# Kernel tuning notes

Hardware: AMD Instinct MI355X
Metric: run time of the kernel (lower is better)

Reference implementation:

```python
import jax, jax.numpy as jnp
import numpy as np

B, T, C, H = 4, 2048, 1024, 16
D = C // H  # head_dim = 64


def setup_inputs() -> dict:
    key = jax.random.key(0)
    ks = jax.random.split(key, 4)
    scale = 1.0 / np.sqrt(C)
    return {
        "x": jax.random.normal(ks[0], (B, T, C), dtype=jnp.float32),
        "attn_mask": jnp.ones((B, T), dtype=jnp.int32),
        "W_qkv": jax.random.normal(ks[1], (C, 3 * C), dtype=jnp.float32) * scale,
        "b_qkv": jnp.zeros((3 * C,), dtype=jnp.float32),
        "W_proj": jax.random.normal(ks[2], (C, C), dtype=jnp.float32) * scale,
        "b_proj": jnp.zeros((C,), dtype=jnp.float32),
    }


def reference(x, attn_mask, W_qkv, b_qkv, W_proj, b_proj):
    b, t, c = x.shape
    qkv = x @ W_qkv + b_qkv                      # (B,T,3C)
    q, k, v = jnp.split(qkv, 3, axis=-1)
    # b t (h d) -> b h t d
    q = q.reshape(b, t, H, D).transpose(0, 2, 1, 3)
    k = k.reshape(b, t, H, D).transpose(0, 2, 1, 3)
    v = v.reshape(b, t, H, D).transpose(0, 2, 1, 3)
    att = jnp.einsum("bhtd,bhsd->bhts", q, k) / jnp.sqrt(jnp.float32(D))
    causal = jnp.tril(jnp.ones((t, t), dtype=bool))[None, None]       # (1,1,T,T)
    pad = (attn_mask[:, None, None, :t] != 0)                         # (B,1,1,T)
    att = jnp.where(causal & pad, att, -jnp.inf)
    att = jax.nn.softmax(att, axis=-1)
    y = jnp.einsum("bhts,bhsd->bhtd", att, v)   # (B,H,T,D)
    y = y.transpose(0, 2, 1, 3).reshape(b, t, c)
    return y @ W_proj + b_proj
```

## Files before the change

kernel.cpp:

```cpp
#include <hip/hip_runtime.h>
#include <math.h>

#define B_ 4
#define T_ 2048
#define C_ 1024
#define H_ 16
#define D_ 64
#define M_ (B_*T_)
#define N1_ (3*C_)

typedef __attribute__((ext_vector_type(8))) short bf16x8;
typedef __attribute__((ext_vector_type(4))) short bf16x4;
typedef __attribute__((ext_vector_type(4))) float f32x4;
typedef __attribute__((ext_vector_type(16))) float f32x16;

__device__ __forceinline__ short f2bf(float f){
  union { float f; unsigned u; } v; v.f = f;
  unsigned r = (v.u + 0x7fffu + ((v.u >> 16) & 1u)) >> 16;
  return (short)r;
}

__device__ __forceinline__ unsigned cvtpk(float lo, float hi){
  unsigned r;
  asm("v_cvt_pk_bf16_f32 %0, %1, %2" : "=v"(r) : "v"(lo), "v"(hi));
  return r;
}

__device__ __forceinline__ void plswap(unsigned &a, unsigned &b){
  asm volatile("v_permlane32_swap_b32 %0, %1" : "+v"(a), "+v"(b));
}
__device__ __forceinline__ float xhalf_add(float x){
  unsigned a = __float_as_uint(x), b = a;
  asm volatile("v_permlane32_swap_b32 %0, %1" : "+v"(a), "+v"(b));
  return __uint_as_float(a) + __uint_as_float(b);
}

__device__ __forceinline__ void gll16(const void* g, void* l){
  __builtin_amdgcn_global_load_lds((const __attribute__((address_space(1))) void*)g,
                                   (__attribute__((address_space(3))) void*)l, 16, 0, 0);
}

__global__ __launch_bounds__(256) void convx(const float* __restrict__ x, short* __restrict__ xb, int n){
  int i = (blockIdx.x*256 + threadIdx.x)*8;
  if (i >= n) return;
  float4 a = *(const float4*)(x+i), b = *(const float4*)(x+i+4);
  bf16x8 o;
  o[0]=f2bf(a.x); o[1]=f2bf(a.y); o[2]=f2bf(a.z); o[3]=f2bf(a.w);
  o[4]=f2bf(b.x); o[5]=f2bf(b.y); o[6]=f2bf(b.z); o[7]=f2bf(b.w);
  *(bf16x8*)(xb+i) = o;
}

__global__ __launch_bounds__(256) void transw(const float* __restrict__ W, short* __restrict__ Wt, int K, int N){
  __shared__ float tl[64][72];
  int tid = threadIdx.x;
  int n0 = blockIdx.x*64, k0 = blockIdx.y*64;
  #pragma unroll
  for (int i=0;i<4;i++){
    int row = (tid>>4) + i*16;
    int col4 = (tid&15)*4;
    float4 v = *(const float4*)&W[(size_t)(k0+row)*N + n0 + col4];
    *(float4*)&tl[row][col4] = v;
  }
  __syncthreads();
  #pragma unroll
  for (int i=0;i<2;i++){
    int nr = (tid>>3) + i*32;
    int ch = tid&7;
    bf16x8 o;
    #pragma unroll
    for (int e=0;e<8;e++) o[e] = f2bf(tl[ch*8+e][nr]);
    *(bf16x8*)&Wt[(size_t)(n0+nr)*K + k0 + ch*8] = o;
  }
}

template<int OUTBF>
__global__ __launch_bounds__(256) void gemm_bt(const short* __restrict__ A, const short* __restrict__ Bt,
           const float* __restrict__ bias, short* __restrict__ outb, float* __restrict__ outf,
           int M, int N, int K)
{
  __shared__ short As[128*32];
  __shared__ short Bs[128*32];
  const int tid = threadIdx.x;
  const int wv = tid >> 6, ln = tid & 63;
  const int lnr = ln & 15, lg = ln >> 4;
  const int m0 = blockIdx.y * 128, n0 = blockIdx.x * 128;
  const int wm = wv >> 1, wn = wv & 1;
  f32x4 acc[4][4];
  #pragma unroll
  for(int i=0;i<4;i++)
    #pragma unroll
    for(int j=0;j<4;j++) acc[i][j] = (f32x4){0.f,0.f,0.f,0.f};

  for (int k0 = 0; k0 < K; k0 += 32){
    #pragma unroll
    for (int c = 0; c < 2; c++){
      int i = c*256 + tid;
      gll16(A  + (size_t)(m0 + (i>>2))*K + k0 + (i&3)*8, (void*)(As + (c*256 + wv*64)*8));
      gll16(Bt + (size_t)(n0 + (i>>2))*K + k0 + (i&3)*8, (void*)(Bs + (c*256 + wv*64)*8));
    }
    __syncthreads();
    bf16x8 af[4], bfr[4];
    #pragma unroll
    for (int mi=0;mi<4;mi++) af[mi]  = *(const bf16x8*)&As[(wm*64 + mi*16 + lnr)*32 + lg*8];
    #pragma unroll
    for (int ni=0;ni<4;ni++) bfr[ni] = *(const bf16x8*)&Bs[(wn*64 + ni*16 + lnr)*32 + lg*8];
    #pragma unroll
    for (int mi=0;mi<4;mi++)
      #pragma unroll
      for (int ni=0;ni<4;ni++)
        acc[mi][ni] = __builtin_amdgcn_mfma_f32_16x16x32_bf16(af[mi], bfr[ni], acc[mi][ni], 0,0,0);
    __syncthreads();
  }

  #pragma unroll
  for (int mi=0;mi<4;mi++){
    #pragma unroll
    for (int ni=0;ni<4;ni++){
      int col = n0 + wn*64 + ni*16 + lnr;
      float bv = bias[col];
      #pragma unroll
      for (int r=0;r<4;r++){
        int row = m0 + wm*64 + mi*16 + lg*4 + r;
        float v = acc[mi][ni][r] + bv;
        if (OUTBF) outb[(size_t)row*N + col] = f2bf(v);
        else       outf[(size_t)row*N + col] = v;
      }
    }
  }
}

__global__ __launch_bounds__(256) void transv(const short* __restrict__ qkv, short* __restrict__ vt){
  __shared__ short tl[64][72];
  int tid = threadIdx.x;
  int t0 = blockIdx.x*64, bh = blockIdx.y;
  int b = bh>>4, h = bh&15;
  int tr = tid>>2, cc = (tid&3)*16;
  const short* src = &qkv[(size_t)(b*T_ + t0 + tr)*N1_ + 2*C_ + h*D_ + cc];
  #pragma unroll
  for (int i=0;i<4;i++){
    bf16x4 v = *(const bf16x4*)(src + i*4);
    *(bf16x4*)&tl[tr][cc + i*4] = v;
  }
  __syncthreads();
  int d = tid>>2, tc = (tid&3)*16;
  #pragma unroll
  for (int i=0;i<2;i++){
    bf16x8 o;
    #pragma unroll
    for (int e=0;e<8;e++) o[e] = tl[tc + i*8 + e][d];
    *(bf16x8*)&vt[(size_t)(bh*D_ + d)*T_ + t0 + tc + i*8] = o;
  }
}

__global__ __launch_bounds__(256) void attn7(const short* __restrict__ qkv, const short* __restrict__ vt,
           const int* __restrict__ mask, short* __restrict__ yb)
{
  __shared__ short Ks[64*64];
  __shared__ short Vs[64*64];
  const int tid = threadIdx.x;
  const int wv = tid>>6, ln = tid&63;
  const int l31 = ln & 31, hi = ln >> 5;
  const int bh = blockIdx.x, b = bh>>4, hd = bh&15;
  const int pr = blockIdx.y;
  const float cexp = 0.18033688f;
  const float MC   = 11.541561f;

  const int srow = tid>>3;
  const int scol = (tid&7) ^ (srow&7);
  int fa[4];
  #pragma unroll
  for (int i=0;i<4;i++)
    fa[i] = l31*128 + ((((i<<1)+hi) ^ (l31&7)) << 4);

  char* ksb = (char*)Ks;
  char* vsb = (char*)Vs;

  #pragma unroll 1
  for (int ph = 0; ph < 2; ph++){
    const int c = ph ? 15 - pr : pr;
    const int q0w = c*128 + wv*32;
    const int ntb  = 2*c + 2;
    const int myNt = 2*c + 1 + (wv>>1);

    bf16x8 qf[4];
    const short* qbase = qkv + (size_t)(b*T_ + q0w + l31)*N1_ + hd*D_ + hi*8;
    #pragma unroll
    for (int ds=0; ds<4; ds++) qf[ds] = *(const bf16x8*)(qbase + ds*16);

    f32x16 o0, o1;
    #pragma unroll
    for (int r=0;r<16;r++){ o0[r]=0.f; o1[r]=0.f; }
    float lsum = 0.f;

    #pragma unroll 1
    for (int jt = 0; jt < ntb; jt++){
      const int j0 = jt << 6;

      int mval = mask[b*T_ + j0 + ln];
      const short* kg = qkv + (size_t)(b*T_ + j0 + srow)*N1_ + C_ + hd*D_ + scol*8;
      const short* vg = vt  + (size_t)((bh<<6) + srow)*T_ + j0 + scol*8;
      gll16(kg,                    ksb + wv*1024);
      gll16(kg + (size_t)32*N1_,   ksb + 4096 + wv*1024);
      gll16(vg,                    vsb + wv*1024);
      gll16(vg + (size_t)32*T_,    vsb + 4096 + wv*1024);
      unsigned long long bm = __ballot(mval != 0);
      __syncthreads();

      if (jt < myNt){
        f32x16 s0, s1;
        #pragma unroll
        for (int r=0;r<16;r++){ s0[r]=0.f; s1[r]=0.f; }
        __builtin_amdgcn_s_setprio(1);
        #pragma unroll
        for (int ds=0; ds<4; ds++){
          bf16x8 k0 = *(const bf16x8*)(ksb + fa[ds]);
          bf16x8 k1 = *(const bf16x8*)(ksb + fa[ds] + 4096);
          s0 = __builtin_amdgcn_mfma_f32_32x32x16_bf16(k0, qf[ds], s0, 0,0,0);
          s1 = __builtin_amdgcn_mfma_f32_32x32x16_bf16(k1, qf[ds], s1, 0,0,0);
        }
        __builtin_amdgcn_s_setprio(0);

        const int qglob = q0w + l31;
        const bool allm = (bm == ~0ull);
        if (!allm){
          #pragma unroll
          for (int r=0;r<16;r++){
            int kr = (r&3) + 8*(r>>2) + 4*hi;
            bool ok0 = (j0 + kr      <= qglob) && ((bm >> kr) & 1);
            bool ok1 = (j0 + kr + 32 <= qglob) && ((bm >> (kr+32)) & 1);
            s0[r] = ok0 ? s0[r] : -INFINITY;
            s1[r] = ok1 ? s1[r] : -INFINITY;
          }
        } else if (j0 + 63 > q0w){
          #pragma unroll
          for (int r=0;r<16;r++){
            int kr = (r&3) + 8*(r>>2) + 4*hi;
            s0[r] = (j0 + kr      <= qglob) ? s0[r] : -INFINITY;
            s1[r] = (j0 + kr + 32 <= qglob) ? s1[r] : -INFINITY;
          }
        }

        #pragma unroll
        for (int r=0;r<16;r++){
          s0[r] = __builtin_amdgcn_exp2f(__builtin_fmaf(s0[r], cexp, -MC));
          s1[r] = __builtin_amdgcn_exp2f(__builtin_fmaf(s1[r], cexp, -MC));
        }
        float u[8];
        #pragma unroll
        for (int i=0;i<8;i++) u[i] = (s0[i]+s0[i+8]) + (s1[i]+s1[i+8]);
        #pragma unroll
        for (int i=0;i<4;i++) u[i] = u[i] + u[i+4];
        float ps = (u[0]+u[1]) + (u[2]+u[3]);
        lsum += xhalf_add(ps);

        unsigned LA[2][4], LB[2][4];
        #pragma unroll
        for (int rq=0; rq<4; rq++){
          LA[0][rq] = cvtpk(s0[4*rq],   s0[4*rq+1]);
          LB[0][rq] = cvtpk(s0[4*rq+2], s0[4*rq+3]);
          LA[1][rq] = cvtpk(s1[4*rq],   s1[4*rq+1]);
          LB[1][rq] = cvtpk(s1[4*rq+2], s1[4*rq+3]);
        }

        #pragma unroll
        for (int kt2=0; kt2<4; kt2++){
          const int kt = kt2>>1, sub = kt2&1;
          bf16x8 v0 = *(const bf16x8*)(vsb + fa[kt2]);
          bf16x8 v1 = *(const bf16x8*)(vsb + fa[kt2] + 4096);
          unsigned a0 = LA[kt][2*sub], a1 = LA[kt][2*sub+1];
          unsigned b0 = LB[kt][2*sub], b1 = LB[kt][2*sub+1];
          plswap(a0, a1);
          plswap(b0, b1);
          union { unsigned u[4]; bf16x8 v; } pf;
          pf.u[0] = a0; pf.u[1] = b0; pf.u[2] = a1; pf.u[3] = b1;
          __builtin_amdgcn_s_setprio(1);
          o0 = __builtin_amdgcn_mfma_f32_32x32x16_bf16(pf.v, v0, o0, 0,0,0);
          o1 = __builtin_amdgcn_mfma_f32_32x32x16_bf16(pf.v, v1, o1, 0,0,0);
          __builtin_amdgcn_s_setprio(0);
        }
      }
      __syncthreads();
    }

    float linv = 1.0f / lsum;
    #pragma unroll
    for (int r=0;r<16;r++){
      int qs = (r&3) + 8*(r>>2) + 4*hi;
      float lv = __shfl(linv, qs);
      size_t base = (size_t)(b*T_ + q0w + qs)*C_ + hd*D_ + l31;
      yb[base]      = f2bf(o0[r]*lv);
      yb[base + 32] = f2bf(o1[r]*lv);
    }
  }
}

extern "C" void kernel_launch(void* const* d_in, const int* in_sizes, int n_in,
                              void* d_out, int out_size, void* d_ws, size_t ws_size,
                              hipStream_t stream){
  const float* x     = (const float*)d_in[0];
  const int*   mask  = (const int*)d_in[1];
  const float* Wqkv  = (const float*)d_in[2];
  const float* bqkv  = (const float*)d_in[3];
  const float* Wproj = (const float*)d_in[4];
  const float* bproj = (const float*)d_in[5];
  float* out = (float*)d_out;

  char* w = (char*)d_ws;
  short* xb     = (short*)w; w += (size_t)M_*C_*2;
  short* wqkvT  = (short*)w; w += (size_t)N1_*C_*2;
  short* wprojT = (short*)w; w += (size_t)C_*C_*2;
  short* qkvb   = (short*)w; w += (size_t)M_*N1_*2;
  short* vtb    = (short*)w; w += (size_t)B_*H_*D_*T_*2;
  short* yb     = (short*)w; w += (size_t)M_*C_*2;

  convx<<<dim3((M_*C_)/(256*8)), 256, 0, stream>>>(x, xb, M_*C_);
  transw<<<dim3(N1_/64, C_/64), 256, 0, stream>>>(Wqkv, wqkvT, C_, N1_);
  transw<<<dim3(C_/64,  C_/64), 256, 0, stream>>>(Wproj, wprojT, C_, C_);
  gemm_bt<1><<<dim3(N1_/128, M_/128), 256, 0, stream>>>(xb, wqkvT, bqkv, qkvb, nullptr, M_, N1_, C_);
  transv<<<dim3(T_/64, B_*H_), 256, 0, stream>>>(qkvb, vtb);
  attn7<<<dim3(B_*H_, 8), 256, 0, stream>>>(qkvb, vtb, mask, yb);
  gemm_bt<0><<<dim3(C_/128, M_/128), 256, 0, stream>>>(yb, wprojT, bproj, nullptr, out, M_, C_, C_);
}
```

Before: 195.4 us.

## Double-buffer attention K/V tiles, swizzle GEMM LDS and workgroup order

The attention kernel now double-buffers the K and V tiles in shared memory and prefetches the next tile and its mask value while the current one is computed, so global loads overlap with MFMA work. The GEMM gets an XOR-swizzled LDS layout to reduce bank conflicts on fragment reads. It also remaps workgroup IDs so that blocks from each group of eight land together, aiming at better L2 reuse. Shared memory for attention doubles, and correctness depends on the sync placement in the unseen loop tail.

```diff
diff --git a/kernel.cpp b/kernel.cpp
--- a/kernel.cpp
+++ b/kernel.cpp
@@ -83,8 +83,25 @@
   const int tid = threadIdx.x;
   const int wv = tid >> 6, ln = tid & 63;
   const int lnr = ln & 15, lg = ln >> 4;
-  const int m0 = blockIdx.y * 128, n0 = blockIdx.x * 128;
+  const int nx = gridDim.x;
+  const int nwg = nx * gridDim.y;
+  const int lin = blockIdx.x + nx * blockIdx.y;
+  const int swz = (lin & 7) * (nwg >> 3) + (lin >> 3);
+  const int m0 = (swz / nx) * 128, n0 = (swz % nx) * 128;
   const int wm = wv >> 1, wn = wv & 1;
+
+  int aoff[4], boff[4];
+  #pragma unroll
+  for (int mi=0;mi<4;mi++){
+    int row = wm*64 + mi*16 + lnr;
+    aoff[mi] = row*64 + ((lg ^ ((row>>1)&3)) << 4);
+  }
+  #pragma unroll
+  for (int ni=0;ni<4;ni++){
+    int row = wn*64 + ni*16 + lnr;
+    boff[ni] = row*64 + ((lg ^ ((row>>1)&3)) << 4);
+  }
+
   f32x4 acc[4][4];
   #pragma unroll
   for(int i=0;i<4;i++)
@@ -95,15 +112,17 @@
     #pragma unroll
     for (int c = 0; c < 2; c++){
       int i = c*256 + tid;
-      gll16(A  + (size_t)(m0 + (i>>2))*K + k0 + (i&3)*8, (void*)(As + (c*256 + wv*64)*8));
-      gll16(Bt + (size_t)(n0 + (i>>2))*K + k0 + (i&3)*8, (void*)(Bs + (c*256 + wv*64)*8));
+      int r = i >> 2;
+      int blk = (i&3) ^ ((r>>1)&3);
+      gll16(A  + (size_t)(m0 + r)*K + k0 + blk*8, (void*)(As + (c*256 + wv*64)*8));
+      gll16(Bt + (size_t)(n0 + r)*K + k0 + blk*8, (void*)(Bs + (c*256 + wv*64)*8));
     }
     __syncthreads();
     bf16x8 af[4], bfr[4];
     #pragma unroll
-    for (int mi=0;mi<4;mi++) af[mi]  = *(const bf16x8*)&As[(wm*64 + mi*16 + lnr)*32 + lg*8];
-    #pragma unroll
-    for (int ni=0;ni<4;ni++) bfr[ni] = *(const bf16x8*)&Bs[(wn*64 + ni*16 + lnr)*32 + lg*8];
+    for (int mi=0;mi<4;mi++) af[mi]  = *(const bf16x8*)((const char*)As + aoff[mi]);
+    #pragma unroll
+    for (int ni=0;ni<4;ni++) bfr[ni] = *(const bf16x8*)((const char*)Bs + boff[ni]);
     #pragma unroll
     for (int mi=0;mi<4;mi++)
       #pragma unroll
@@ -152,11 +171,11 @@
   }
 }
 
-__global__ __launch_bounds__(256) void attn7(const short* __restrict__ qkv, const short* __restrict__ vt,
+__global__ __launch_bounds__(256) void attn8(const short* __restrict__ qkv, const short* __restrict__ vt,
            const int* __restrict__ mask, short* __restrict__ yb)
 {
-  __shared__ short Ks[64*64];
-  __shared__ short Vs[64*64];
+  __shared__ short Ks[2][64*64];
+  __shared__ short Vs[2][64*64];
   const int tid = threadIdx.x;
   const int wv = tid>>6, ln = tid&63;
   const int l31 = ln & 31, hi = ln >> 5;
@@ -167,13 +186,12 @@
 
   const int srow = tid>>3;
   const int scol = (tid&7) ^ (srow&7);
+  const short* kgb = qkv + (size_t)(b*T_ + srow)*N1_ + C_ + hd*D_ + scol*8;
+  const short* vgb = vt  + (size_t)((bh<<6) + srow)*T_ + scol*8;
   int fa[4];
   #pragma unroll
   for (int i=0;i<4;i++)
     fa[i] = l31*128 + ((((i<<1)+hi) ^ (l31&7)) << 4);
-
-  char* ksb = (char*)Ks;
-  char* vsb = (char*)Vs;
 
   #pragma unroll 1
   for (int ph = 0; ph < 2; ph++){
@@ -192,21 +210,35 @@
     for (int r=0;r<16;r++){ o0[r]=0.f; o1[r]=0.f; }
     float lsum = 0.f;
 
+    int mv_next = mask[b*T_ + ln];
+    {
+      char* kd = (char*)Ks[0]; char* vd = (char*)Vs[0];
+      gll16(kgb,                  kd + wv*1024);
+      gll16(kgb + (size_t)32*N1_, kd + 4096 + wv*1024);
+      gll16(vgb,                  vd + wv*1024);
+      gll16(vgb + (size_t)32*T_,  vd + 4096 + wv*1024);
+    }
+    __syncthreads();
+
     #pragma unroll 1
     for (int jt = 0; jt < ntb; jt++){
       const int j0 = jt << 6;
-
-      int mval = mask[b*T_ + j0 + ln];
-      const short* kg = qkv + (size_t)(b*T_ + j0 + srow)*N1_ + C_ + hd*D_ + scol*8;
-      const short* vg = vt  + (size_t)((bh<<6) + srow)*T_ + j0 + scol*8;
-      gll16(kg,                    ksb + wv*1024);
-      gll16(kg + (size_t)32*N1_,   ksb + 4096 + wv*1024);
-      gll16(vg,                    vsb + wv*1024);
-      gll16(vg + (size_t)32*T_,    vsb + 4096 + wv*1024);
-      unsigned long long bm = __ballot(mval != 0);
-      __syncthreads();
+      int mv_cur = mv_next;
+      if (jt+1 < ntb){
+        mv_next = mask[b*T_ + ((jt+1)<<6) + ln];
+        char* kd = (char*)Ks[(jt+1)&1]; char* vd = (char*)Vs[(jt+1)&1];
+        const short* kg = kgb + (size_t)((jt+1)<<6)*N1_;
+        const short* vg = vgb + ((jt+1)<<6);
+        gll16(kg,                  kd + wv*1024);
+        gll16(kg + (size_t)32*N1_, kd + 4096 + wv*1024);
+        gll16(vg,                  vd + wv*1024);
+        gll16(vg + (size_t)32*T_,  vd + 4096 + wv*1024);
+      }
+      unsigned long long bm = __ballot(mv_cur != 0);
 
       if (jt < myNt){
+        const char* ksb = (const char*)Ks[jt&1];
+        const char* vsb = (const char*)Vs[jt&1];
         f32x16 s0, s1;
         #pragma unroll
         for (int r=0;r<16;r++){ s0[r]=0.f; s1[r]=0.f; }
@@ -318,6 +350,6 @@
   transw<<<dim3(C_/64,  C_/64), 256, 0, stream>>>(Wproj, wprojT, C_, C_);
   gemm_bt<1><<<dim3(N1_/128, M_/128), 256, 0, stream>>>(xb, wqkvT, bqkv, qkvb, nullptr, M_, N1_, C_);
   transv<<<dim3(T_/64, B_*H_), 256, 0, stream>>>(qkvb, vtb);
-  attn7<<<dim3(B_*H_, 8), 256, 0, stream>>>(qkvb, vtb, mask, yb);
+  attn8<<<dim3(B_*H_, 8), 256, 0, stream>>>(qkvb, vtb, mask, yb);
   gemm_bt<0><<<dim3(C_/128, M_/128), 256, 0, stream>>>(yb, wprojT, bproj, nullptr, out, M_, C_, C_);
 }
```

After: 192.9 us. Within noise of the previous version (-1.2%).
